# Performance work log

Measured on AMD Instinct MI355X. Metric: run time of the kernel, lower is better.

The kernel has to match this reference:

```python
import jax, jax.numpy as jnp
import numpy as np

B, T, D, H = 4, 2048, 1024, 16
HD = D // H  # head_dim = 64

def setup_inputs() -> dict:
    key = jax.random.key(0)
    k1, k2, k3 = jax.random.split(key, 3)
    s = 1.0 / np.sqrt(D)
    return {
        "x": jax.random.normal(k1, (B, T, D), dtype=jnp.float32),
        "w_qkv": jax.random.normal(k2, (D, 3 * D), dtype=jnp.float32) * s,
        "b_qkv": jnp.zeros((3 * D,), dtype=jnp.float32),
        "w_proj": jax.random.normal(k3, (D, D), dtype=jnp.float32) * s,
        "b_proj": jnp.zeros((D,), dtype=jnp.float32),
    }

def reference(x, w_qkv, b_qkv, w_proj, b_proj):
    b, t, c = x.shape
    qkv = x @ w_qkv + b_qkv                       # [B,T,3D]
    qkv = qkv.reshape(b, t, 3, H, HD)
    q, k, v = (jnp.transpose(qkv[:, :, i], (0, 2, 1, 3)) for i in range(3))  # [B,H,T,HD]
    scale = 1.0 / np.sqrt(HD)
    attn = jnp.einsum('bhqd,bhkd->bhqk', q, k) * scale  # [B,H,T,T]
    attn = jax.nn.softmax(attn, axis=-1)
    out = jnp.einsum('bhqk,bhkd->bhqd', attn, v)        # [B,H,T,HD]
    out = jnp.transpose(out, (0, 2, 1, 3)).reshape(b, t, c)
    return out @ w_proj + b_proj
```

## Files before the change

### kernel.cpp

```cpp
#include <hip/hip_runtime.h>
#include <hip/hip_bf16.h>

#define T_SEQ   2048
#define D_MODEL 1024
#define N_HEADS 16
#define HEAD_DIM 64
#define BT      8192
#define N3D     3072

using short8  = __attribute__((ext_vector_type(8))) short;
using short4v = __attribute__((ext_vector_type(4))) short;
using floatx4 = __attribute__((ext_vector_type(4))) float;

#define QSCALE 0.18033688f

__device__ __forceinline__ unsigned short rne_bf16(float f) {
  unsigned int u = __float_as_uint(f);
  u = (u + 0x7fffu + ((u >> 16) & 1u)) >> 16;
  return (unsigned short)u;
}

__device__ __forceinline__ void gload_lds16(const unsigned short* g,
                                            unsigned short* l) {
  __builtin_amdgcn_global_load_lds(
      (const __attribute__((address_space(1))) void*)g,
      (__attribute__((address_space(3))) void*)l, 16, 0, 0);
}

__device__ __forceinline__ void transpose_tile(const float* __restrict__ in,
                                               unsigned short* __restrict__ out_hi,
                                               int R, int C, int bid) {
  __shared__ float tile[64][65];
  int tiles_c = C >> 6;
  int r0 = (bid / tiles_c) << 6;
  int c0 = (bid % tiles_c) << 6;
  int tid = threadIdx.x;
#pragma unroll
  for (int i = 0; i < 16; ++i) {
    int idx = tid + i * 256;
    int r = idx >> 6, c = idx & 63;
    tile[r][c] = in[(size_t)(r0 + r) * C + c0 + c];
  }
  __syncthreads();
#pragma unroll
  for (int i = 0; i < 16; ++i) {
    int idx = tid + i * 256;
    int orow = idx >> 6, oc = idx & 63;
    out_hi[(size_t)(c0 + orow) * R + r0 + oc] = rne_bf16(tile[oc][orow]);
  }
}

__global__ __launch_bounds__(256) void k_prep(
    const float* __restrict__ x, unsigned short* __restrict__ x_bf,
    const float* __restrict__ wqkv, unsigned short* __restrict__ wq_T,
    const float* __restrict__ wproj, unsigned short* __restrict__ wp_T) {
  int bid = blockIdx.x;
  if (bid < 4096) {
    size_t i = ((size_t)bid * 256 + threadIdx.x) * 8;
    float4 a = *(const float4*)(x + i);
    float4 b = *(const float4*)(x + i + 4);
    short8 v;
    v[0] = (short)rne_bf16(a.x); v[1] = (short)rne_bf16(a.y);
    v[2] = (short)rne_bf16(a.z); v[3] = (short)rne_bf16(a.w);
    v[4] = (short)rne_bf16(b.x); v[5] = (short)rne_bf16(b.y);
    v[6] = (short)rne_bf16(b.z); v[7] = (short)rne_bf16(b.w);
    *(short8*)(((short*)x_bf) + i) = v;
  } else if (bid < 4096 + 768) {
    transpose_tile(wqkv, wq_T, 1024, 3072, bid - 4096);
  } else {
    transpose_tile(wproj, wp_T, 1024, 1024, bid - 4096 - 768);
  }
}

__global__ __launch_bounds__(256) void k_qkv_gemm(
    const unsigned short* __restrict__ A, const unsigned short* __restrict__ Bt,
    const float* __restrict__ bias,
    unsigned short* __restrict__ Qo, unsigned short* __restrict__ Ko,
    unsigned short* __restrict__ Vt) {
  __shared__ __align__(16) unsigned short As[128 * 64];
  __shared__ __align__(16) unsigned short Bs[128 * 64];
  int tid = threadIdx.x;
  int wg = (blockIdx.x & 7) * 192 + (blockIdx.x >> 3);
  int m0 = (wg / 24) * 128;
  int n0 = (wg % 24) * 128;
  int which = n0 >> 10;
  int w = tid >> 6, lane = tid & 63, quad = lane >> 4, l16 = lane & 15;
  int wm = (w >> 1) * 64, wn = (w & 1) * 64;
  floatx4 acc[4][4] = {};

  int r0 = tid >> 3;
  int gsh = (((tid & 7) ^ (r0 & 7)) << 3);

  int a_off[4][2], b_off[4][2];
#pragma unroll
  for (int t = 0; t < 4; ++t) {
    int ra = wm + t * 16 + l16, rb = wn + t * 16 + l16;
#pragma unroll
    for (int ks = 0; ks < 2; ++ks) {
      a_off[t][ks] = ra * 64 + (((ks * 4 + quad) ^ (ra & 7)) << 3);
      b_off[t][ks] = rb * 64 + (((ks * 4 + quad) ^ (rb & 7)) << 3);
    }
  }

  for (int k0 = 0; k0 < 1024; k0 += 64) {
#pragma unroll
    for (int i = 0; i < 4; ++i) {
      int sub = (tid & ~63) + i * 256;
      gload_lds16(A + (size_t)(m0 + r0 + i * 32) * 1024 + k0 + gsh,
                  &As[sub * 8]);
      gload_lds16(Bt + (size_t)(n0 + r0 + i * 32) * 1024 + k0 + gsh,
                  &Bs[sub * 8]);
    }
    __syncthreads();
#pragma unroll
    for (int ks = 0; ks < 2; ++ks) {
      short8 af[4], bfr[4];
#pragma unroll
      for (int mt = 0; mt < 4; ++mt) af[mt] = *(const short8*)(&As[a_off[mt][ks]]);
#pragma unroll
      for (int nt = 0; nt < 4; ++nt) bfr[nt] = *(const short8*)(&Bs[b_off[nt][ks]]);
      if (which == 2) {
#pragma unroll
        for (int mt = 0; mt < 4; ++mt)
#pragma unroll
          for (int nt = 0; nt < 4; ++nt)
            acc[mt][nt] = __builtin_amdgcn_mfma_f32_16x16x32_bf16(af[mt], bfr[nt],
                                                                  acc[mt][nt], 0, 0, 0);
      } else {
#pragma unroll
        for (int mt = 0; mt < 4; ++mt)
#pragma unroll
          for (int nt = 0; nt < 4; ++nt)
            acc[mt][nt] = __builtin_amdgcn_mfma_f32_16x16x32_bf16(bfr[nt], af[mt],
                                                                  acc[mt][nt], 0, 0, 0);
      }
    }
    __syncthreads();
  }

  if (which == 2) {
#pragma unroll
    for (int nt = 0; nt < 4; ++nt) {
      int n = n0 + wn + nt * 16 + l16;
      float bv = bias[n];
      int nn = n & 1023;
      int h = nn >> 6, hd = nn & 63;
#pragma unroll
      for (int mt = 0; mt < 4; ++mt) {
        int mbase = m0 + wm + mt * 16 + quad * 4;
        int b = mbase >> 11;
        int t0 = mbase & 2047;
        int head = b * N_HEADS + h;
        short4v vv;
#pragma unroll
        for (int r = 0; r < 4; ++r) vv[r] = (short)rne_bf16(acc[mt][nt][r] + bv);
        *(short4v*)(&Vt[((size_t)head * HEAD_DIM + hd) * T_SEQ + t0]) = vv;
      }
    }
  } else {
    unsigned short* dst = (which == 0) ? Qo : Ko;
    float scl = (which == 0) ? QSCALE : 1.0f;
#pragma unroll
    for (int nt = 0; nt < 4; ++nt) {
      int nbase = n0 + wn + nt * 16 + quad * 4;
      int nn = nbase & 1023;
      int h = nn >> 6, hd0 = nn & 63;
      float4 bv4 = *(const float4*)(&bias[nbase]);
#pragma unroll
      for (int mt = 0; mt < 4; ++mt) {
        int m = m0 + wm + mt * 16 + l16;
        int b = m >> 11;
        int t = m & 2047;
        int head = b * N_HEADS + h;
        short4v ov;
        ov[0] = (short)rne_bf16((acc[mt][nt][0] + bv4.x) * scl);
        ov[1] = (short)rne_bf16((acc[mt][nt][1] + bv4.y) * scl);
        ov[2] = (short)rne_bf16((acc[mt][nt][2] + bv4.z) * scl);
        ov[3] = (short)rne_bf16((acc[mt][nt][3] + bv4.w) * scl);
        *(short4v*)(&dst[((size_t)head * T_SEQ + t) * HEAD_DIM + hd0]) = ov;
      }
    }
  }
}

__global__ __launch_bounds__(512, 4) void k_attn(
    const unsigned short* __restrict__ Q, const unsigned short* __restrict__ K,
    const unsigned short* __restrict__ Vt, unsigned short* __restrict__ Oo) {
  __shared__ __align__(16) unsigned short Klds[2][64 * 64];
  __shared__ __align__(16) unsigned short Vlds[3][64 * 64];
  int tid = threadIdx.x;
  int head = ((blockIdx.x & 7) << 3) + (blockIdx.x >> 6);
  int qb = ((blockIdx.x >> 3) & 7) << 8;
  int b = head >> 4, h = head & 15;
  int w = tid >> 6, lane = tid & 63, quad = lane >> 4, l16 = lane & 15;
  const unsigned short* Qh = Q + (size_t)head * T_SEQ * HEAD_DIM;
  const unsigned short* Kh = K + (size_t)head * T_SEQ * HEAD_DIM;
  const unsigned short* Vh = Vt + (size_t)head * HEAD_DIM * T_SEQ;

  short8 qf[2][2];
#pragma unroll
  for (int qi = 0; qi < 2; ++qi) {
    int qrow = qb + w * 32 + qi * 16 + l16;
#pragma unroll
    for (int ks = 0; ks < 2; ++ks)
      qf[qi][ks] = *(const short8*)(Qh + (size_t)qrow * 64 + ks * 32 + quad * 8);
  }

  short8 ones;
#pragma unroll
  for (int j = 0; j < 8; ++j) ones[j] = (short)0x3F80;

  floatx4 O[2][4] = {};
  floatx4 Osum[2] = {};
  const floatx4 zf = {};

  int sg = tid >> 6;
  int xs = lane ^ sg;
  int ntp = xs >> 4, mp = xs & 15;
  int ksrc = ((ntp >> 1) << 5) + ((mp >> 2) << 3) + ((ntp & 1) << 2) + (mp & 3);
  int vsrc = xs;
  int sub = tid & ~63;

  int pu[2][4];
#pragma unroll
  for (int ks = 0; ks < 2; ++ks) {
    int gk = ks * 4 + quad;
#pragma unroll
    for (int t = 0; t < 4; ++t)
      pu[ks][t] = (((gk << 6) + t * 16 + l16) ^ gk) << 3;
  }

  auto stageK = [&](unsigned short* dst, int kb) {
    gload_lds16(Kh + ((size_t)(kb * 64 + ksrc)) * 64 + sg * 8, dst + sub * 8);
  };
  auto stageV = [&](unsigned short* dst, int kb) {
    gload_lds16(Vh + (size_t)vsrc * T_SEQ + kb * 64 + sg * 8, dst + sub * 8);
  };

  short8 pPrev[2][2];

  auto qk = [&](const unsigned short* Kb_, floatx4 (&s)[2][4]) {
#pragma unroll
    for (int ks = 0; ks < 2; ++ks) {
#pragma unroll
      for (int nt = 0; nt < 4; ++nt) {
        short8 kf = *(const short8*)(Kb_ + pu[ks][nt]);
        if (ks == 0) {
          s[0][nt] = __builtin_amdgcn_mfma_f32_16x16x32_bf16(kf, qf[0][0], zf, 0, 0, 0);
          s[1][nt] = __builtin_amdgcn_mfma_f32_16x16x32_bf16(kf, qf[1][0], zf, 0, 0, 0);
        } else {
          s[0][nt] = __builtin_amdgcn_mfma_f32_16x16x32_bf16(kf, qf[0][1], s[0][nt], 0, 0, 0);
          s[1][nt] = __builtin_amdgcn_mfma_f32_16x16x32_bf16(kf, qf[1][1], s[1][nt], 0, 0, 0);
        }
      }
    }
  };

  auto pv = [&](const unsigned short* Vb_) {
#pragma unroll
    for (int ks = 0; ks < 2; ++ks) {
      Osum[0] = __builtin_amdgcn_mfma_f32_16x16x32_bf16(ones, pPrev[0][ks], Osum[0], 0, 0, 0);
      Osum[1] = __builtin_amdgcn_mfma_f32_16x16x32_bf16(ones, pPrev[1][ks], Osum[1], 0, 0, 0);
#pragma unroll
      for (int dt = 0; dt < 4; ++dt) {
        short8 vf = *(const short8*)(Vb_ + pu[ks][dt]);
        O[0][dt] = __builtin_amdgcn_mfma_f32_16x16x32_bf16(vf, pPrev[0][ks], O[0][dt], 0, 0, 0);
        O[1][dt] = __builtin_amdgcn_mfma_f32_16x16x32_bf16(vf, pPrev[1][ks], O[1][dt], 0, 0, 0);
      }
    }
  };

  auto expPack = [&](floatx4 (&s)[2][4]) {
#pragma unroll
    for (int qi = 0; qi < 2; ++qi) {
      unsigned int dw[4][2];
#pragma unroll
      for (int nt = 0; nt < 4; ++nt) {
        float p0 = __builtin_amdgcn_exp2f(s[qi][nt][0]);
        float p1 = __builtin_amdgcn_exp2f(s[qi][nt][1]);
        float p2 = __builtin_amdgcn_exp2f(s[qi][nt][2]);
        float p3 = __builtin_amdgcn_exp2f(s[qi][nt][3]);
        __hip_bfloat162 lo2 = __float22bfloat162_rn(make_float2(p0, p1));
        __hip_bfloat162 hi2 = __float22bfloat162_rn(make_float2(p2, p3));
        dw[nt][0] = *(unsigned int*)&lo2;
        dw[nt][1] = *(unsigned int*)&hi2;
      }
#pragma unroll
      for (int ks = 0; ks < 2; ++ks) {
        union { unsigned int u[4]; short8 s8; } cv;
        cv.u[0] = dw[2 * ks][0];
        cv.u[1] = dw[2 * ks][1];
        cv.u[2] = dw[2 * ks + 1][0];
        cv.u[3] = dw[2 * ks + 1][1];
        pPrev[qi][ks] = cv.s8;
      }
    }
  };

  unsigned short* Kcur = &Klds[1][0];
  unsigned short* Koth = &Klds[0][0];
  unsigned short* Vp = &Vlds[0][0];
  unsigned short* Vc = &Vlds[1][0];
  unsigned short* Vn = &Vlds[2][0];

  stageK(Koth, 0); stageV(Vp, 0);
  __syncthreads();
  stageK(Kcur, 1); stageV(Vc, 1);
  {
    floatx4 s[2][4];
    qk(Koth, s);
    expPack(s);
  }
  __syncthreads();

#pragma unroll 1
  for (int t = 1; t < 32; ++t) {
    if (t < 31) { stageK(Koth, t + 1); stageV(Vn, t + 1); }
    floatx4 s[2][4];
    __builtin_amdgcn_s_setprio(1);
    qk(Kcur, s);
    pv(Vp);
    __builtin_amdgcn_s_setprio(0);
    expPack(s);
    __syncthreads();
    unsigned short* tk = Kcur; Kcur = Koth; Koth = tk;
    unsigned short* tv = Vp; Vp = Vc; Vc = Vn; Vn = tv;
  }
  pv(Vp);

#pragma unroll
  for (int qi = 0; qi < 2; ++qi) {
    float inv = 1.0f / Osum[qi][0];
    int t = qb + w * 32 + qi * 16 + l16;
    size_t rowo = ((size_t)(b * T_SEQ + t)) * D_MODEL + h * HEAD_DIM;
#pragma unroll
    for (int dt = 0; dt < 4; ++dt) {
      short4v ov;
#pragma unroll
      for (int r = 0; r < 4; ++r) ov[r] = (short)rne_bf16(O[qi][dt][r] * inv);
      *(short4v*)(&Oo[rowo + dt * 16 + quad * 4]) = ov;
    }
  }
}

__global__ __launch_bounds__(256) void k_proj_gemm(
    const unsigned short* __restrict__ A, const unsigned short* __restrict__ Bt,
    const float* __restrict__ bias, float* __restrict__ out) {
  __shared__ __align__(16) unsigned short As[128 * 64];
  __shared__ __align__(16) unsigned short Bs[128 * 64];
  int tid = threadIdx.x;
  int wg = (blockIdx.x & 7) * 64 + (blockIdx.x >> 3);
  int m0 = (wg >> 3) * 128;
  int n0 = (wg & 7) * 128;
  int w = tid >> 6, lane = tid & 63, quad = lane >> 4, l16 = lane & 15;
  int wm = (w >> 1) * 64, wn = (w & 1) * 64;
  floatx4 acc[4][4] = {};

  int r0 = tid >> 3;
  int gsh = (((tid & 7) ^ (r0 & 7)) << 3);

  int a_off[4][2], b_off[4][2];
#pragma unroll
  for (int t = 0; t < 4; ++t) {
    int ra = wm + t * 16 + l16, rb = wn + t * 16 + l16;
#pragma unroll
    for (int ks = 0; ks < 2; ++ks) {
      a_off[t][ks] = ra * 64 + (((ks * 4 + quad) ^ (ra & 7)) << 3);
      b_off[t][ks] = rb * 64 + (((ks * 4 + quad) ^ (rb & 7)) << 3);
    }
  }

  for (int k0 = 0; k0 < 1024; k0 += 64) {
#pragma unroll
    for (int i = 0; i < 4; ++i) {
      int sub = (tid & ~63) + i * 256;
      gload_lds16(A + (size_t)(m0 + r0 + i * 32) * 1024 + k0 + gsh,
                  &As[sub * 8]);
      gload_lds16(Bt + (size_t)(n0 + r0 + i * 32) * 1024 + k0 + gsh,
                  &Bs[sub * 8]);
    }
    __syncthreads();
#pragma unroll
    for (int ks = 0; ks < 2; ++ks) {
      short8 af[4], bfr[4];
#pragma unroll
      for (int mt = 0; mt < 4; ++mt) af[mt] = *(const short8*)(&As[a_off[mt][ks]]);
#pragma unroll
      for (int nt = 0; nt < 4; ++nt) bfr[nt] = *(const short8*)(&Bs[b_off[nt][ks]]);
#pragma unroll
      for (int mt = 0; mt < 4; ++mt)
#pragma unroll
        for (int nt = 0; nt < 4; ++nt)
          acc[mt][nt] = __builtin_amdgcn_mfma_f32_16x16x32_bf16(bfr[nt], af[mt],
                                                                acc[mt][nt], 0, 0, 0);
    }
    __syncthreads();
  }

#pragma unroll
  for (int nt = 0; nt < 4; ++nt) {
    int nbase = n0 + wn + nt * 16 + quad * 4;
    float4 bv4 = *(const float4*)(&bias[nbase]);
#pragma unroll
    for (int mt = 0; mt < 4; ++mt) {
      int m = m0 + wm + mt * 16 + l16;
      float4 o;
      o.x = acc[mt][nt][0] + bv4.x;
      o.y = acc[mt][nt][1] + bv4.y;
      o.z = acc[mt][nt][2] + bv4.z;
      o.w = acc[mt][nt][3] + bv4.w;
      *(float4*)(&out[(size_t)m * 1024 + nbase]) = o;
    }
  }
}

extern "C" void kernel_launch(void* const* d_in, const int* in_sizes, int n_in,
                              void* d_out, int out_size, void* d_ws, size_t ws_size,
                              hipStream_t stream) {
  const float* x     = (const float*)d_in[0];
  const float* wqkv  = (const float*)d_in[1];
  const float* bqkv  = (const float*)d_in[2];
  const float* wproj = (const float*)d_in[3];
  const float* bproj = (const float*)d_in[4];

  char* ws = (char*)d_ws;
  size_t off = 0;
  unsigned short* x_bf  = (unsigned short*)(ws + off); off += (size_t)BT * D_MODEL * 2;
  unsigned short* wq_T  = (unsigned short*)(ws + off); off += (size_t)N3D * D_MODEL * 2;
  unsigned short* wp_T  = (unsigned short*)(ws + off); off += (size_t)D_MODEL * D_MODEL * 2;
  unsigned short* Qb    = (unsigned short*)(ws + off); off += (size_t)BT * D_MODEL * 2;
  unsigned short* Kb    = (unsigned short*)(ws + off); off += (size_t)BT * D_MODEL * 2;
  unsigned short* Vt    = (unsigned short*)(ws + off); off += (size_t)BT * D_MODEL * 2;
  unsigned short* a_bf  = (unsigned short*)(ws + off); off += (size_t)BT * D_MODEL * 2;

  k_prep<<<5120, 256, 0, stream>>>(x, x_bf, wqkv, wq_T, wproj, wp_T);
  k_qkv_gemm<<<(BT / 128) * (N3D / 128), 256, 0, stream>>>(x_bf, wq_T, bqkv, Qb, Kb, Vt);
  k_attn<<<512, 512, 0, stream>>>(Qb, Kb, Vt, a_bf);
  k_proj_gemm<<<(BT / 128) * (D_MODEL / 128), 256, 0, stream>>>(a_bf, wp_T, bproj, (float*)d_out);
}
```

Before: 274.1 us.

## Split attention key range across two half-blocks and merge partial outputs in LDS

The attention kernel now launches 1024 threads per block. Each 512-thread half processes half of the key/value sequence with its own double- and triple-buffered LDS region. Because the softmax has no running max, the two halves' partial O and row sums are combined through shared memory, and half 0 normalizes and writes the output. The aim is more waves per CU for latency hiding and a shorter serial loop per block. In exchange it adds a final LDS reduction and larger LDS use per block, and the tighter launch bounds may constrain registers.

Result: slower. 744.6 us (+171.7%).

```diff
diff --git a/kernel.cpp b/kernel.cpp
--- a/kernel.cpp
+++ b/kernel.cpp
@@ -183,24 +183,27 @@
   }
 }
 
-__global__ __launch_bounds__(512, 4) void k_attn(
+__global__ __launch_bounds__(1024, 8) void k_attn(
     const unsigned short* __restrict__ Q, const unsigned short* __restrict__ K,
     const unsigned short* __restrict__ Vt, unsigned short* __restrict__ Oo) {
-  __shared__ __align__(16) unsigned short Klds[2][64 * 64];
-  __shared__ __align__(16) unsigned short Vlds[3][64 * 64];
+  __shared__ __align__(16) unsigned short smemAll[40960];
   int tid = threadIdx.x;
+  int half = tid >> 9;
+  int htid = tid & 511;
   int head = ((blockIdx.x & 7) << 3) + (blockIdx.x >> 6);
   int qb = ((blockIdx.x >> 3) & 7) << 8;
   int b = head >> 4, h = head & 15;
-  int w = tid >> 6, lane = tid & 63, quad = lane >> 4, l16 = lane & 15;
+  int wq = (tid >> 6) & 7, lane = tid & 63, quad = lane >> 4, l16 = lane & 15;
   const unsigned short* Qh = Q + (size_t)head * T_SEQ * HEAD_DIM;
-  const unsigned short* Kh = K + (size_t)head * T_SEQ * HEAD_DIM;
-  const unsigned short* Vh = Vt + (size_t)head * HEAD_DIM * T_SEQ;
+  const unsigned short* Kh = K + (size_t)head * T_SEQ * HEAD_DIM
+                               + (size_t)(half * 1024) * HEAD_DIM;
+  const unsigned short* Vh = Vt + (size_t)head * HEAD_DIM * T_SEQ
+                               + half * 1024;
 
   short8 qf[2][2];
 #pragma unroll
   for (int qi = 0; qi < 2; ++qi) {
-    int qrow = qb + w * 32 + qi * 16 + l16;
+    int qrow = qb + wq * 32 + qi * 16 + l16;
 #pragma unroll
     for (int ks = 0; ks < 2; ++ks)
       qf[qi][ks] = *(const short8*)(Qh + (size_t)qrow * 64 + ks * 32 + quad * 8);
@@ -214,12 +217,12 @@
   floatx4 Osum[2] = {};
   const floatx4 zf = {};
 
-  int sg = tid >> 6;
+  int sg = htid >> 6;
   int xs = lane ^ sg;
   int ntp = xs >> 4, mp = xs & 15;
   int ksrc = ((ntp >> 1) << 5) + ((mp >> 2) << 3) + ((ntp & 1) << 2) + (mp & 3);
   int vsrc = xs;
-  int sub = tid & ~63;
+  int sub = htid & ~63;
 
   int pu[2][4];
 #pragma unroll
@@ -297,11 +300,12 @@
     }
   };
 
-  unsigned short* Kcur = &Klds[1][0];
-  unsigned short* Koth = &Klds[0][0];
-  unsigned short* Vp = &Vlds[0][0];
-  unsigned short* Vc = &Vlds[1][0];
-  unsigned short* Vn = &Vlds[2][0];
+  unsigned short* hbase = smemAll + half * 20480;
+  unsigned short* Kcur = hbase + 4096;
+  unsigned short* Koth = hbase;
+  unsigned short* Vp = hbase + 8192;
+  unsigned short* Vc = hbase + 12288;
+  unsigned short* Vn = hbase + 16384;
 
   stageK(Koth, 0); stageV(Vp, 0);
   __syncthreads();
@@ -314,8 +318,8 @@
   __syncthreads();
 
 #pragma unroll 1
-  for (int t = 1; t < 32; ++t) {
-    if (t < 31) { stageK(Koth, t + 1); stageV(Vn, t + 1); }
+  for (int t = 1; t < 16; ++t) {
+    if (t < 15) { stageK(Koth, t + 1); stageV(Vn, t + 1); }
     floatx4 s[2][4];
     __builtin_amdgcn_s_setprio(1);
     qk(Kcur, s);
@@ -328,17 +332,36 @@
   }
   pv(Vp);
 
-#pragma unroll
-  for (int qi = 0; qi < 2; ++qi) {
-    float inv = 1.0f / Osum[qi][0];
-    int t = qb + w * 32 + qi * 16 + l16;
-    size_t rowo = ((size_t)(b * T_SEQ + t)) * D_MODEL + h * HEAD_DIM;
-#pragma unroll
-    for (int dt = 0; dt < 4; ++dt) {
-      short4v ov;
-#pragma unroll
-      for (int r = 0; r < 4; ++r) ov[r] = (short)rne_bf16(O[qi][dt][r] * inv);
-      *(short4v*)(&Oo[rowo + dt * 16 + quad * 4]) = ov;
+  __syncthreads();
+  float* cO = (float*)smemAll;
+  float* cS = cO + 16384;
+  if (half == 1) {
+#pragma unroll
+    for (int qi = 0; qi < 2; ++qi) {
+      cS[htid * 2 + qi] = Osum[qi][0];
+#pragma unroll
+      for (int dt = 0; dt < 4; ++dt)
+#pragma unroll
+        for (int r = 0; r < 4; ++r)
+          cO[htid * 32 + qi * 16 + dt * 4 + r] = O[qi][dt][r];
+    }
+  }
+  __syncthreads();
+  if (half == 0) {
+#pragma unroll
+    for (int qi = 0; qi < 2; ++qi) {
+      float inv = 1.0f / (Osum[qi][0] + cS[htid * 2 + qi]);
+      int t = qb + wq * 32 + qi * 16 + l16;
+      size_t rowo = ((size_t)(b * T_SEQ + t)) * D_MODEL + h * HEAD_DIM;
+#pragma unroll
+      for (int dt = 0; dt < 4; ++dt) {
+        short4v ov;
+#pragma unroll
+        for (int r = 0; r < 4; ++r)
+          ov[r] = (short)rne_bf16(
+              (O[qi][dt][r] + cO[htid * 32 + qi * 16 + dt * 4 + r]) * inv);
+        *(short4v*)(&Oo[rowo + dt * 16 + quad * 4]) = ov;
+      }
     }
   }
 }
@@ -435,6 +458,6 @@
 
   k_prep<<<5120, 256, 0, stream>>>(x, x_bf, wqkv, wq_T, wproj, wp_T);
   k_qkv_gemm<<<(BT / 128) * (N3D / 128), 256, 0, stream>>>(x_bf, wq_T, bqkv, Qb, Kb, Vt);
-  k_attn<<<512, 512, 0, stream>>>(Qb, Kb, Vt, a_bf);
+  k_attn<<<512, 1024, 0, stream>>>(Qb, Kb, Vt, a_bf);
   k_proj_gemm<<<(BT / 128) * (D_MODEL / 128), 256, 0, stream>>>(a_bf, wp_T, bproj, (float*)d_out);
 }
```
